# Kernel optimization log

Measured on AMD Instinct MI355X. Metric: run time of the kernel, lower is better.

Reference implementation:

```python
import jax, jax.numpy as jnp
import numpy as np

N_NODES = 100000
N_EDGES = 1600000
N_GRAPHS = 64
IN_F, HID, OUT_F = 10, 128, 101


def setup_inputs() -> dict:
    key = jax.random.key(0)
    ks = jax.random.split(key, 12)
    x = jax.random.normal(ks[0], (N_NODES, IN_F), dtype=jnp.float32)
    edge_index = jax.random.randint(ks[1], (2, N_EDGES), 0, N_NODES, dtype=jnp.int64)
    batch = jnp.sort(jax.random.randint(ks[2], (N_NODES,), 0, N_GRAPHS, dtype=jnp.int64))
    def lin(k, fi, fo):
        s = 1.0 / np.sqrt(fi)
        return jax.random.uniform(k, (fi, fo), minval=-s, maxval=s, dtype=jnp.float32)
    W1 = lin(ks[3], IN_F, HID); b1 = jnp.zeros((HID,), jnp.float32)
    W2 = lin(ks[4], HID, HID); b2 = jnp.zeros((HID,), jnp.float32)
    W3 = lin(ks[5], HID, HID); b3 = jnp.zeros((HID,), jnp.float32)
    Wl = lin(ks[6], HID, OUT_F)
    bl = jax.random.uniform(ks[7], (OUT_F,), minval=-1/np.sqrt(HID), maxval=1/np.sqrt(HID), dtype=jnp.float32)
    return {"x": x, "edge_index": edge_index, "batch": batch,
            "W1": W1, "b1": b1, "W2": W2, "b2": b2, "W3": W3, "b3": b3,
            "Wl": Wl, "bl": bl}


def _gcn_norm(edge_index, n_nodes):
    # Add self-loops and compute symmetric normalization (PyG gcn_norm).
    loop = jnp.arange(n_nodes, dtype=edge_index.dtype)
    src = jnp.concatenate([edge_index[0], loop])
    dst = jnp.concatenate([edge_index[1], loop])
    deg = jax.ops.segment_sum(jnp.ones_like(dst, dtype=jnp.float32), dst, num_segments=n_nodes)
    dis = jnp.where(deg > 0, jax.lax.rsqrt(deg), 0.0)
    w = dis[src] * dis[dst]  # [E + N]
    return src, dst, w


def _gcn_conv(x, W, b, src, dst, w, n_nodes):
    h = x @ W                      # transform first (matches GCNConv)
    msg = h[src] * w[:, None]      # gather + edge normalize
    out = jax.ops.segment_sum(msg, dst, num_segments=n_nodes)  # scatter-add
    return out + b


def reference(x, edge_index, batch, W1, b1, W2, b2, W3, b3, Wl, bl):
    n = x.shape[0]
    src, dst, w = _gcn_norm(edge_index, n)
    h = jax.nn.relu(_gcn_conv(x, W1, b1, src, dst, w, n))
    h = jax.nn.relu(_gcn_conv(h, W2, b2, src, dst, w, n))
    h = _gcn_conv(h, W3, b3, src, dst, w, n)
    # global mean pool per graph
    sums = jax.ops.segment_sum(h, batch, num_segments=N_GRAPHS)
    cnts = jax.ops.segment_sum(jnp.ones((n,), jnp.float32), batch, num_segments=N_GRAPHS)
    pooled = sums / jnp.maximum(cnts, 1.0)[:, None]
    # dropout is identity in eval mode
    return pooled @ Wl + bl
```

## Files before the change

### kernel.cpp

```cpp
#include <hip/hip_runtime.h>
#include <hip/hip_bf16.h>

#define HID 128
#define OUTF 101
#define INF 10
#define XPAD 16

#define BUCK_SHIFT 8
#define NBUCK_MAX 512
#define BCAP 4608
#define FS_EPT 18
#define BS_TPB 256
#define BS_EPT 32
#define BS_EPB (BS_TPB * BS_EPT)

typedef __hip_bfloat16 bf16;
typedef __attribute__((ext_vector_type(8))) short short8;
typedef __attribute__((ext_vector_type(4))) float f32x4;

__device__ __forceinline__ float bflo(unsigned u) { return __uint_as_float(u << 16); }
__device__ __forceinline__ float bfhi(unsigned u) { return __uint_as_float(u & 0xffff0000u); }
__device__ __forceinline__ unsigned pk2(float a, float b) {
    __hip_bfloat162 t;
    t.x = __float2bfloat16(a);
    t.y = __float2bfloat16(b);
    return *reinterpret_cast<unsigned*>(&t);
}


__device__ __forceinline__ void wsplit_body(const float* __restrict__ W, bf16* __restrict__ wfh,
                                            bf16* __restrict__ wfl, int t) {
    int j    = t & 7;
    int lane = (t >> 3) & 63;
    int nt   = (t >> 9) & 7;
    int kb   = t >> 12;
    int k  = kb * 32 + (lane >> 4) * 8 + j;
    int nn = nt * 16 + (lane & 15);
    float w = W[k * HID + nn];
    float hi = __bfloat162float(__float2bfloat16(w));
    wfh[t] = __float2bfloat16(hi);
    wfl[t] = __float2bfloat16(w - hi);
}

__global__ void prep_kernel(const float* __restrict__ x, float* __restrict__ xp, int n,
                            const float* __restrict__ W2, bf16* __restrict__ wf2h,
                            bf16* __restrict__ wf2l,
                            const float* __restrict__ W3, bf16* __restrict__ wf3h,
                            bf16* __restrict__ wf3l,
                            int* __restrict__ gcur, int nbuck,
                            float* __restrict__ sums, int sums_n,
                            int nb_xpad) {
    int b = blockIdx.x;
    int tid = threadIdx.x;
    if (b < nb_xpad) {
        int t = b * 256 + tid;
        if (t < n * XPAD) {
            int i = t >> 4;
            int f = t & 15;
            xp[t] = (f < INF) ? x[(size_t)i * INF + f] : 0.f;
        }
        return;
    }
    b -= nb_xpad;
    if (b < 64) { wsplit_body(W2, wf2h, wf2l, b * 256 + tid); return; }
    b -= 64;
    if (b < 64) { wsplit_body(W3, wf3h, wf3l, b * 256 + tid); return; }
    b -= 64;
    if (b == 0) {
        for (int k = tid; k < nbuck; k += 256) gcur[k] = k * BCAP;
        return;
    }
    b -= 1;
    {
        int t = b * 256 + tid;
        if (t * 4 < sums_n) ((float4*)sums)[t] = make_float4(0.f, 0.f, 0.f, 0.f);
    }
}


__global__ __launch_bounds__(BS_TPB) void bucket_scatter_kernel(
        const int* __restrict__ src, const int* __restrict__ dst, int E,
        int* __restrict__ gcur, int2* __restrict__ estage, int nbuck) {
    __shared__ int cnt[NBUCK_MAX];
    __shared__ int base[NBUCK_MAX];
    int tid = threadIdx.x;
    int e0 = blockIdx.x * BS_EPB + tid;
    int ds[BS_EPT], ss[BS_EPT];
#pragma unroll
    for (int t = 0; t < BS_EPT; ++t) {
        int e = e0 + t * BS_TPB;
        ds[t] = (e < E) ? dst[e] : -1;
        ss[t] = (e < E) ? src[e] : 0;
    }
    for (int b = tid; b < NBUCK_MAX; b += BS_TPB) cnt[b] = 0;
    __syncthreads();
#pragma unroll
    for (int t = 0; t < BS_EPT; ++t)
        if (ds[t] >= 0) atomicAdd(&cnt[ds[t] >> BUCK_SHIFT], 1);
    __syncthreads();
    for (int b = tid; b < nbuck; b += BS_TPB) {
        int c = cnt[b];
        base[b] = c ? atomicAdd(&gcur[b], c) : 0;
    }
    __syncthreads();
    for (int b = tid; b < NBUCK_MAX; b += BS_TPB) cnt[b] = 0;
    __syncthreads();
#pragma unroll
    for (int t = 0; t < BS_EPT; ++t)
        if (ds[t] >= 0) {
            int bk = ds[t] >> BUCK_SHIFT;
            int o = atomicAdd(&cnt[bk], 1);
            estage[base[bk] + o] = make_int2(ss[t], ds[t]);
        }
}

__global__ __launch_bounds__(NBUCK_MAX) void scanb_kernel(const int* __restrict__ gcur,
                                                          int* __restrict__ bbase,
                                                          int* __restrict__ rowp,
                                                          int nbuck, int N) {
    __shared__ int sh[NBUCK_MAX];
    int t = threadIdx.x;
    sh[t] = (t < nbuck) ? (gcur[t] - t * BCAP) : 0;
    __syncthreads();
    for (int off = 1; off < NBUCK_MAX; off <<= 1) {
        int v = (t >= off) ? sh[t - off] : 0;
        __syncthreads();
        sh[t] += v;
        __syncthreads();
    }
    if (t < nbuck) bbase[t] = (t == 0) ? 0 : sh[t - 1];
    if (t == 0) {
        bbase[nbuck] = sh[nbuck - 1];
        rowp[N] = sh[nbuck - 1];
    }
}

__global__ __launch_bounds__(BS_TPB) void fine_scatter_kernel(
        const int2* __restrict__ estage, const int* __restrict__ bbase,
        float* __restrict__ dis, int* __restrict__ rowp,
        int* __restrict__ csrs, int n) {
    __shared__ int hist[256];
    __shared__ int pfx[256];
    __shared__ int lcur[256];
    int b = blockIdx.x;
    int tid = threadIdx.x;
    int node_lo = b << BUCK_SHIFT;
    int bb = bbase[b];
    int cnt = bbase[b + 1] - bb;
    int slo = b * BCAP;
    int2 regs[FS_EPT];
#pragma unroll
    for (int t = 0; t < FS_EPT; ++t) {
        int k = tid + t * BS_TPB;
        regs[t] = (k < cnt) ? estage[slo + k] : make_int2(0, -1);
    }
    hist[tid] = 0;
    __syncthreads();
#pragma unroll
    for (int t = 0; t < FS_EPT; ++t)
        if (regs[t].y >= 0) atomicAdd(&hist[regs[t].y & 255], 1);
    __syncthreads();
    int deg = hist[tid];
    int node = node_lo + tid;
    if (node < n) dis[node] = rsqrtf((float)(deg + 1));
    pfx[tid] = deg;
    __syncthreads();
    for (int off = 1; off < 256; off <<= 1) {
        int v = (tid >= off) ? pfx[tid - off] : 0;
        __syncthreads();
        pfx[tid] += v;
        __syncthreads();
    }
    int excl = (tid == 0) ? 0 : pfx[tid - 1];
    if (node < n) rowp[node] = bb + excl;
    lcur[tid] = excl;
    __syncthreads();
#pragma unroll
    for (int t = 0; t < FS_EPT; ++t)
        if (regs[t].y >= 0) {
            int pos = bb + atomicAdd(&lcur[regs[t].y & 255], 1);
            csrs[pos] = regs[t].x;
        }
}

__global__ __launch_bounds__(256) void aggxform10_kernel(
        const float* __restrict__ xp, const int* __restrict__ rowp,
        const int* __restrict__ csrs, const float* __restrict__ dis,
        const float* __restrict__ W1, const float* __restrict__ b1,
        bf16* __restrict__ h, int n) {
    int i = blockIdx.x * 4 + (threadIdx.x >> 6);
    if (i >= n) return;
    int lane = threadIdx.x & 63;
    int slot = lane >> 4;
    int f = lane & 15;
    float dd = dis[i];

    float acc = (slot == 0) ? xp[(size_t)i * XPAD + f] * dd : 0.f;
    int beg = rowp[i];
    int end = rowp[i + 1];
    for (int base = beg; base < end; base += 4) {
        int e = base + slot;
        int idx = (e < end) ? e : end - 1;
        int s = csrs[idx];
        float w = (e < end) ? dis[s] : 0.f;
        acc = fmaf(xp[(size_t)s * XPAD + f], w, acc);
    }
    acc += __shfl_xor(acc, 16, 64);
    acc += __shfl_xor(acc, 32, 64);
    acc *= dd;

    float axk[INF];
#pragma unroll
    for (int k = 0; k < INF; ++k) axk[k] = __shfl(acc, k, 16);

    int j0 = 2 * lane;
    float2 bb = *(const float2*)(b1 + j0);
    float r0 = bb.x, r1 = bb.y;
#pragma unroll
    for (int k = 0; k < INF; ++k) {
        float2 wv = *(const float2*)(W1 + k * HID + j0);
        r0 = fmaf(axk[k], wv.x, r0);
        r1 = fmaf(axk[k], wv.y, r1);
    }
    r0 = fmaxf(r0, 0.f);
    r1 = fmaxf(r1, 0.f);
    ((unsigned*)(h + (size_t)i * HID))[lane] = pk2(r0, r1);
}


__global__ __launch_bounds__(256) void lin128_mfma_kernel(
        const bf16* __restrict__ in, const bf16* __restrict__ wfh,
        const bf16* __restrict__ wfl, bf16* __restrict__ out, int n) {
    __shared__ short8 wh[2048];
    __shared__ short8 wl[2048];
    for (int v = threadIdx.x; v < 2048; v += 256) {
        wh[v] = ((const short8*)wfh)[v];
        wl[v] = ((const short8*)wfl)[v];
    }
    __syncthreads();

    int lane = threadIdx.x & 63;
    int wave = threadIdx.x >> 6;
    int col = lane & 15;
    int quad = lane >> 4;
    int m0 = blockIdx.x * 128 + wave * 32;

    f32x4 acc[2][8];
#pragma unroll
    for (int mt = 0; mt < 2; ++mt)
#pragma unroll
        for (int nt = 0; nt < 8; ++nt) acc[mt][nt] = (f32x4){0.f, 0.f, 0.f, 0.f};

    long rmax = n - 1;
    long r0 = m0 + col;        if (r0 > rmax) r0 = rmax;
    long r1 = m0 + 16 + col;   if (r1 > rmax) r1 = rmax;

#pragma unroll
    for (int kb = 0; kb < 4; ++kb) {
        int kofs = kb * 32 + quad * 8;
        short8 a0 = *(const short8*)(in + r0 * HID + kofs);
        short8 a1 = *(const short8*)(in + r1 * HID + kofs);
        int bbase = kb * 512 + lane;
#pragma unroll
        for (int nt = 0; nt < 8; ++nt) {
            short8 bh = wh[bbase + nt * 64];
            short8 bl = wl[bbase + nt * 64];
            acc[0][nt] = __builtin_amdgcn_mfma_f32_16x16x32_bf16(a0, bh, acc[0][nt], 0, 0, 0);
            acc[1][nt] = __builtin_amdgcn_mfma_f32_16x16x32_bf16(a1, bh, acc[1][nt], 0, 0, 0);
            acc[0][nt] = __builtin_amdgcn_mfma_f32_16x16x32_bf16(a0, bl, acc[0][nt], 0, 0, 0);
            acc[1][nt] = __builtin_amdgcn_mfma_f32_16x16x32_bf16(a1, bl, acc[1][nt], 0, 0, 0);
        }
    }

#pragma unroll
    for (int mt = 0; mt < 2; ++mt) {
        int mb = m0 + mt * 16 + quad * 4;
#pragma unroll
        for (int r = 0; r < 4; ++r) {
            int m = mb + r;
            if (m < n) {
                bf16* orow = out + (size_t)m * HID + col;
#pragma unroll
                for (int nt = 0; nt < 8; ++nt)
                    orow[nt * 16] = __float2bfloat16(acc[mt][nt][r]);
            }
        }
    }
}

__global__ __launch_bounds__(256) void agg128_kernel(
        const bf16* __restrict__ h, const int* __restrict__ rowp,
        const int* __restrict__ csrs, const float* __restrict__ dis,
        const float* __restrict__ b, bf16* __restrict__ out, int n, int relu) {
    int i = blockIdx.x * 4 + (threadIdx.x >> 6);
    if (i >= n) return;
    int lane = threadIdx.x & 63;
    int slot = lane >> 4;
    int f = lane & 15;
    float dd = dis[i];

    float acc[8];
    if (slot == 0) {
        uint4 v = *(const uint4*)(h + (size_t)i * HID + f * 8);
        acc[0] = bflo(v.x) * dd; acc[1] = bfhi(v.x) * dd;
        acc[2] = bflo(v.y) * dd; acc[3] = bfhi(v.y) * dd;
        acc[4] = bflo(v.z) * dd; acc[5] = bfhi(v.z) * dd;
        acc[6] = bflo(v.w) * dd; acc[7] = bfhi(v.w) * dd;
    } else {
#pragma unroll
        for (int j = 0; j < 8; ++j) acc[j] = 0.f;
    }

    int beg = rowp[i];
    int end = rowp[i + 1];
    for (int base = beg; base < end; base += 8) {
        int e0 = base + slot;
        int e1 = base + 4 + slot;
        int i0 = (e0 < end) ? e0 : end - 1;
        int i1 = (e1 < end) ? e1 : end - 1;
        int s0 = csrs[i0];
        int s1 = csrs[i1];
        float w0 = (e0 < end) ? dis[s0] : 0.f;
        float w1 = (e1 < end) ? dis[s1] : 0.f;
        uint4 v0 = *(const uint4*)(h + (size_t)s0 * HID + f * 8);
        uint4 v1 = *(const uint4*)(h + (size_t)s1 * HID + f * 8);
        acc[0] = fmaf(bflo(v0.x), w0, acc[0]); acc[1] = fmaf(bfhi(v0.x), w0, acc[1]);
        acc[2] = fmaf(bflo(v0.y), w0, acc[2]); acc[3] = fmaf(bfhi(v0.y), w0, acc[3]);
        acc[4] = fmaf(bflo(v0.z), w0, acc[4]); acc[5] = fmaf(bfhi(v0.z), w0, acc[5]);
        acc[6] = fmaf(bflo(v0.w), w0, acc[6]); acc[7] = fmaf(bfhi(v0.w), w0, acc[7]);
        acc[0] = fmaf(bflo(v1.x), w1, acc[0]); acc[1] = fmaf(bfhi(v1.x), w1, acc[1]);
        acc[2] = fmaf(bflo(v1.y), w1, acc[2]); acc[3] = fmaf(bfhi(v1.y), w1, acc[3]);
        acc[4] = fmaf(bflo(v1.z), w1, acc[4]); acc[5] = fmaf(bfhi(v1.z), w1, acc[5]);
        acc[6] = fmaf(bflo(v1.w), w1, acc[6]); acc[7] = fmaf(bfhi(v1.w), w1, acc[7]);
    }

#pragma unroll
    for (int j = 0; j < 8; ++j) {
        acc[j] += __shfl_xor(acc[j], 16, 64);
        acc[j] += __shfl_xor(acc[j], 32, 64);
    }

    float4 b0 = *(const float4*)(b + f * 8);
    float4 b1 = *(const float4*)(b + f * 8 + 4);
    float r[8];
    r[0] = fmaf(acc[0], dd, b0.x); r[1] = fmaf(acc[1], dd, b0.y);
    r[2] = fmaf(acc[2], dd, b0.z); r[3] = fmaf(acc[3], dd, b0.w);
    r[4] = fmaf(acc[4], dd, b1.x); r[5] = fmaf(acc[5], dd, b1.y);
    r[6] = fmaf(acc[6], dd, b1.z); r[7] = fmaf(acc[7], dd, b1.w);
    if (relu) {
#pragma unroll
        for (int j = 0; j < 8; ++j) r[j] = fmaxf(r[j], 0.f);
    }
    if (slot == 0) {
        uint4 pk;
        pk.x = pk2(r[0], r[1]);
        pk.y = pk2(r[2], r[3]);
        pk.z = pk2(r[4], r[5]);
        pk.w = pk2(r[6], r[7]);
        *(uint4*)(out + (size_t)i * HID + f * 8) = pk;
    }
}


__global__ void pool_kernel(const bf16* __restrict__ h, const int* __restrict__ batch, int n,
                            float* __restrict__ sums) {
    int g = blockIdx.x;
    int j = threadIdx.x;
    int lo = 0, hi = n;
    while (lo < hi) { int mid = (lo + hi) >> 1; if (batch[mid] < g) lo = mid + 1; else hi = mid; }
    int start = lo;
    lo = start; hi = n;
    while (lo < hi) { int mid = (lo + hi) >> 1; if (batch[mid] < g + 1) lo = mid + 1; else hi = mid; }
    int end = lo;
    float acc = 0.f;
    for (int i = start + blockIdx.y; i < end; i += gridDim.y)
        acc += __bfloat162float(h[(size_t)i * HID + j]);
    atomicAdd(&sums[g * HID + j], acc);
}

__global__ void final_kernel(const float* __restrict__ sums, const int* __restrict__ batch, int n,
                             const float* __restrict__ Wl, const float* __restrict__ bl,
                             float* __restrict__ out) {
    int g = blockIdx.x;
    int o = threadIdx.x;
    __shared__ float p[HID];
    int lo = 0, hi = n;
    while (lo < hi) { int mid = (lo + hi) >> 1; if (batch[mid] < g) lo = mid + 1; else hi = mid; }
    int start = lo;
    lo = start; hi = n;
    while (lo < hi) { int mid = (lo + hi) >> 1; if (batch[mid] < g + 1) lo = mid + 1; else hi = mid; }
    float cnt = fmaxf((float)(lo - start), 1.0f);
    p[o] = sums[g * HID + o] / cnt;
    __syncthreads();
    if (o < OUTF) {
        float acc = bl[o];
#pragma unroll 8
        for (int k = 0; k < HID; ++k) acc += p[k] * Wl[k * OUTF + o];
        out[g * OUTF + o] = acc;
    }
}


extern "C" void kernel_launch(void* const* d_in, const int* in_sizes, int n_in,
                              void* d_out, int out_size, void* d_ws, size_t ws_size,
                              hipStream_t stream) {
    const float* x   = (const float*)d_in[0];
    const int*   ei  = (const int*)d_in[1];
    const int*   bat = (const int*)d_in[2];
    const float* W1  = (const float*)d_in[3];
    const float* b1  = (const float*)d_in[4];
    const float* W2  = (const float*)d_in[5];
    const float* b2  = (const float*)d_in[6];
    const float* W3  = (const float*)d_in[7];
    const float* b3  = (const float*)d_in[8];
    const float* Wl  = (const float*)d_in[9];
    const float* bl  = (const float*)d_in[10];

    const int N = in_sizes[0] / INF;
    const int E = in_sizes[1] / 2;
    const int G = out_size / OUTF;
    const int* src = ei;
    const int* dst = ei + E;

    const int nbuck = (N + (1 << BUCK_SHIFT) - 1) >> BUCK_SHIFT;

    char* w = (char*)d_ws;
    bf16*  bufA   = (bf16*)w;  w += (size_t)N * HID * 2;
    bf16*  bufB   = (bf16*)w;  w += (size_t)N * HID * 2;
    float* dis    = (float*)w; w += (size_t)N * 4;
    int*   rowp   = (int*)w;   w += (size_t)(N + 8) * 4;
    int*   csrs   = (int*)w;   w += (size_t)E * 4;
    float* sums   = (float*)w; w += (size_t)G * HID * 4;
    int*   gcur   = (int*)w;   w += (size_t)(nbuck + 8) * 4;
    int*   bbase  = (int*)w;   w += (size_t)(nbuck + 8) * 4;
    bf16*  wf2h   = (bf16*)w;  w += (size_t)HID * HID * 2;
    bf16*  wf2l   = (bf16*)w;  w += (size_t)HID * HID * 2;
    bf16*  wf3h   = (bf16*)w;  w += (size_t)HID * HID * 2;
    bf16*  wf3l   = (bf16*)w;  w += (size_t)HID * HID * 2;
    int2*  estage = (int2*)bufA;
    float* xp     = (float*)bufB;

    const int nb_xpad = (N * XPAD + 255) / 256;
    const int sums_n = G * HID;
    prep_kernel<<<nb_xpad + 64 + 64 + 1 + 8, 256, 0, stream>>>(
        x, xp, N, W2, wf2h, wf2l, W3, wf3h, wf3l, gcur, nbuck, sums, sums_n, nb_xpad);

    bucket_scatter_kernel<<<(E + BS_EPB - 1) / BS_EPB, BS_TPB, 0, stream>>>(src, dst, E, gcur,
                                                                            estage, nbuck);
    scanb_kernel<<<1, NBUCK_MAX, 0, stream>>>(gcur, bbase, rowp, nbuck, N);
    fine_scatter_kernel<<<nbuck, BS_TPB, 0, stream>>>(estage, bbase, dis, rowp, csrs, N);

    aggxform10_kernel<<<(N + 3) / 4, 256, 0, stream>>>(xp, rowp, csrs, dis, W1, b1, bufA, N);
    lin128_mfma_kernel<<<(N + 127) / 128, 256, 0, stream>>>(bufA, wf2h, wf2l, bufB, N);
    agg128_kernel<<<(N + 3) / 4, 256, 0, stream>>>(bufB, rowp, csrs, dis, b2, bufA, N, 1);
    lin128_mfma_kernel<<<(N + 127) / 128, 256, 0, stream>>>(bufA, wf3h, wf3l, bufB, N);
    agg128_kernel<<<(N + 3) / 4, 256, 0, stream>>>(bufB, rowp, csrs, dis, b3, bufA, N, 0);

    pool_kernel<<<dim3(G, 32), HID, 0, stream>>>(bufA, bat, N, sums);
    final_kernel<<<G, HID, 0, stream>>>(sums, bat, N, Wl, bl, (float*)d_out);
}
```

Measured before the change: 387.7 us.

## Pre-scale source features by degree norm to drop per-edge dis gathers

Folds the source-side normalization dis[s] into the features before aggregation: x is scaled in fine_scatter and the MFMA output rows are scaled by dis[m]. The aggregation loops can then skip the per-edge dis[s] gather and use plain adds. A zero dummy row at index N replaces masked weights for out-of-range edges. The aggregation loops are also widened (more edges per iteration, float4 loads for the 10-feature layer), and the separate x-padding pass is merged into fine_scatter. The cost is one extra multiply per output element in the linear kernel and slightly larger buffers.

Measured after the change: 356.5 us. 8.1% less time.

```diff
diff --git a/kernel.cpp b/kernel.cpp
--- a/kernel.cpp
+++ b/kernel.cpp
@@ -42,26 +42,17 @@
     wfl[t] = __float2bfloat16(w - hi);
 }
 
-__global__ void prep_kernel(const float* __restrict__ x, float* __restrict__ xp, int n,
-                            const float* __restrict__ W2, bf16* __restrict__ wf2h,
+__global__ void prep_kernel(const float* __restrict__ W2, bf16* __restrict__ wf2h,
                             bf16* __restrict__ wf2l,
                             const float* __restrict__ W3, bf16* __restrict__ wf3h,
                             bf16* __restrict__ wf3l,
                             int* __restrict__ gcur, int nbuck,
                             float* __restrict__ sums, int sums_n,
-                            int nb_xpad) {
+                            float* __restrict__ xps_dummy,
+                            unsigned* __restrict__ hs_dummy)
+{
     int b = blockIdx.x;
     int tid = threadIdx.x;
-    if (b < nb_xpad) {
-        int t = b * 256 + tid;
-        if (t < n * XPAD) {
-            int i = t >> 4;
-            int f = t & 15;
-            xp[t] = (f < INF) ? x[(size_t)i * INF + f] : 0.f;
-        }
-        return;
-    }
-    b -= nb_xpad;
     if (b < 64) { wsplit_body(W2, wf2h, wf2l, b * 256 + tid); return; }
     b -= 64;
     if (b < 64) { wsplit_body(W3, wf3h, wf3l, b * 256 + tid); return; }
@@ -71,10 +62,13 @@
         return;
     }
     b -= 1;
-    {
+    if (b < 8) {
         int t = b * 256 + tid;
         if (t * 4 < sums_n) ((float4*)sums)[t] = make_float4(0.f, 0.f, 0.f, 0.f);
-    }
+        return;
+    }
+    if (tid < XPAD) xps_dummy[tid] = 0.f;
+    if (tid < 64) hs_dummy[tid] = 0u;
 }
 
 
@@ -138,10 +132,12 @@
 __global__ __launch_bounds__(BS_TPB) void fine_scatter_kernel(
         const int2* __restrict__ estage, const int* __restrict__ bbase,
         float* __restrict__ dis, int* __restrict__ rowp,
-        int* __restrict__ csrs, int n) {
+        int* __restrict__ csrs, const float* __restrict__ x,
+        float* __restrict__ xps, int n) {
     __shared__ int hist[256];
     __shared__ int pfx[256];
     __shared__ int lcur[256];
+    __shared__ float sdis[256];
     int b = blockIdx.x;
     int tid = threadIdx.x;
     int node_lo = b << BUCK_SHIFT;
@@ -162,7 +158,9 @@
     __syncthreads();
     int deg = hist[tid];
     int node = node_lo + tid;
-    if (node < n) dis[node] = rsqrtf((float)(deg + 1));
+    float dv = rsqrtf((float)(deg + 1));
+    sdis[tid] = dv;
+    if (node < n) dis[node] = dv;
     pfx[tid] = deg;
     __syncthreads();
     for (int off = 1; off < 256; off <<= 1) {
@@ -181,37 +179,66 @@
             int pos = bb + atomicAdd(&lcur[regs[t].y & 255], 1);
             csrs[pos] = regs[t].x;
         }
+#pragma unroll
+    for (int t = 0; t < 16; ++t) {
+        int idx = tid + t * 256;
+        int nd = node_lo + (idx >> 4);
+        int f = idx & 15;
+        if (nd < n)
+            xps[(size_t)nd * XPAD + f] = (f < INF) ? x[(size_t)nd * INF + f] * sdis[idx >> 4] : 0.f;
+    }
 }
 
 __global__ __launch_bounds__(256) void aggxform10_kernel(
-        const float* __restrict__ xp, const int* __restrict__ rowp,
+        const float* __restrict__ xps, const int* __restrict__ rowp,
         const int* __restrict__ csrs, const float* __restrict__ dis,
         const float* __restrict__ W1, const float* __restrict__ b1,
         bf16* __restrict__ h, int n) {
     int i = blockIdx.x * 4 + (threadIdx.x >> 6);
     if (i >= n) return;
     int lane = threadIdx.x & 63;
-    int slot = lane >> 4;
-    int f = lane & 15;
+    int slot = lane >> 2;
+    int c = lane & 3;
     float dd = dis[i];
 
-    float acc = (slot == 0) ? xp[(size_t)i * XPAD + f] * dd : 0.f;
+    float acc[4];
+    if (slot == 0) {
+        float4 v = *(const float4*)(xps + (size_t)i * XPAD + c * 4);
+        acc[0] = v.x; acc[1] = v.y; acc[2] = v.z; acc[3] = v.w;
+    } else {
+        acc[0] = acc[1] = acc[2] = acc[3] = 0.f;
+    }
+
     int beg = rowp[i];
     int end = rowp[i + 1];
-    for (int base = beg; base < end; base += 4) {
-        int e = base + slot;
-        int idx = (e < end) ? e : end - 1;
-        int s = csrs[idx];
-        float w = (e < end) ? dis[s] : 0.f;
-        acc = fmaf(xp[(size_t)s * XPAD + f], w, acc);
-    }
-    acc += __shfl_xor(acc, 16, 64);
-    acc += __shfl_xor(acc, 32, 64);
-    acc *= dd;
+    for (int base = beg; base < end; base += 32) {
+        int e0 = base + slot;
+        int e1 = base + 16 + slot;
+        int i0 = (e0 < end) ? e0 : end - 1;
+        int i1 = (e1 < end) ? e1 : end - 1;
+        int s0 = csrs[i0];
+        int s1 = csrs[i1];
+        s0 = (e0 < end) ? s0 : n;
+        s1 = (e1 < end) ? s1 : n;
+        float4 v0 = *(const float4*)(xps + (size_t)s0 * XPAD + c * 4);
+        float4 v1 = *(const float4*)(xps + (size_t)s1 * XPAD + c * 4);
+        acc[0] += v0.x + v1.x;
+        acc[1] += v0.y + v1.y;
+        acc[2] += v0.z + v1.z;
+        acc[3] += v0.w + v1.w;
+    }
+#pragma unroll
+    for (int j = 0; j < 4; ++j) {
+        acc[j] += __shfl_xor(acc[j], 4, 64);
+        acc[j] += __shfl_xor(acc[j], 8, 64);
+        acc[j] += __shfl_xor(acc[j], 16, 64);
+        acc[j] += __shfl_xor(acc[j], 32, 64);
+        acc[j] *= dd;
+    }
 
     float axk[INF];
 #pragma unroll
-    for (int k = 0; k < INF; ++k) axk[k] = __shfl(acc, k, 16);
+    for (int k = 0; k < INF; ++k) axk[k] = __shfl(acc[k & 3], k >> 2, 4);
 
     int j0 = 2 * lane;
     float2 bb = *(const float2*)(b1 + j0);
@@ -230,7 +257,8 @@
 
 __global__ __launch_bounds__(256) void lin128_mfma_kernel(
         const bf16* __restrict__ in, const bf16* __restrict__ wfh,
-        const bf16* __restrict__ wfl, bf16* __restrict__ out, int n) {
+        const bf16* __restrict__ wfl, const float* __restrict__ dis,
+        bf16* __restrict__ out, int n) {
     __shared__ short8 wh[2048];
     __shared__ short8 wl[2048];
     for (int v = threadIdx.x; v < 2048; v += 256) {
@@ -279,17 +307,18 @@
         for (int r = 0; r < 4; ++r) {
             int m = mb + r;
             if (m < n) {
+                float dm = dis[m];
                 bf16* orow = out + (size_t)m * HID + col;
 #pragma unroll
                 for (int nt = 0; nt < 8; ++nt)
-                    orow[nt * 16] = __float2bfloat16(acc[mt][nt][r]);
+                    orow[nt * 16] = __float2bfloat16(acc[mt][nt][r] * dm);
             }
         }
     }
 }
 
 __global__ __launch_bounds__(256) void agg128_kernel(
-        const bf16* __restrict__ h, const int* __restrict__ rowp,
+        const bf16* __restrict__ hs, const int* __restrict__ rowp,
         const int* __restrict__ csrs, const float* __restrict__ dis,
         const float* __restrict__ b, bf16* __restrict__ out, int n, int relu) {
     int i = blockIdx.x * 4 + (threadIdx.x >> 6);
@@ -301,11 +330,11 @@
 
     float acc[8];
     if (slot == 0) {
-        uint4 v = *(const uint4*)(h + (size_t)i * HID + f * 8);
-        acc[0] = bflo(v.x) * dd; acc[1] = bfhi(v.x) * dd;
-        acc[2] = bflo(v.y) * dd; acc[3] = bfhi(v.y) * dd;
-        acc[4] = bflo(v.z) * dd; acc[5] = bfhi(v.z) * dd;
-        acc[6] = bflo(v.w) * dd; acc[7] = bfhi(v.w) * dd;
+        uint4 v = *(const uint4*)(hs + (size_t)i * HID + f * 8);
+        acc[0] = bflo(v.x); acc[1] = bfhi(v.x);
+        acc[2] = bflo(v.y); acc[3] = bfhi(v.y);
+        acc[4] = bflo(v.z); acc[5] = bfhi(v.z);
+        acc[6] = bflo(v.w); acc[7] = bfhi(v.w);
     } else {
 #pragma unroll
         for (int j = 0; j < 8; ++j) acc[j] = 0.f;
@@ -313,25 +342,25 @@
 
     int beg = rowp[i];
     int end = rowp[i + 1];
-    for (int base = beg; base < end; base += 8) {
-        int e0 = base + slot;
-        int e1 = base + 4 + slot;
-        int i0 = (e0 < end) ? e0 : end - 1;
-        int i1 = (e1 < end) ? e1 : end - 1;
-        int s0 = csrs[i0];
-        int s1 = csrs[i1];
-        float w0 = (e0 < end) ? dis[s0] : 0.f;
-        float w1 = (e1 < end) ? dis[s1] : 0.f;
-        uint4 v0 = *(const uint4*)(h + (size_t)s0 * HID + f * 8);
-        uint4 v1 = *(const uint4*)(h + (size_t)s1 * HID + f * 8);
-        acc[0] = fmaf(bflo(v0.x), w0, acc[0]); acc[1] = fmaf(bfhi(v0.x), w0, acc[1]);
-        acc[2] = fmaf(bflo(v0.y), w0, acc[2]); acc[3] = fmaf(bfhi(v0.y), w0, acc[3]);
-        acc[4] = fmaf(bflo(v0.z), w0, acc[4]); acc[5] = fmaf(bfhi(v0.z), w0, acc[5]);
-        acc[6] = fmaf(bflo(v0.w), w0, acc[6]); acc[7] = fmaf(bfhi(v0.w), w0, acc[7]);
-        acc[0] = fmaf(bflo(v1.x), w1, acc[0]); acc[1] = fmaf(bfhi(v1.x), w1, acc[1]);
-        acc[2] = fmaf(bflo(v1.y), w1, acc[2]); acc[3] = fmaf(bfhi(v1.y), w1, acc[3]);
-        acc[4] = fmaf(bflo(v1.z), w1, acc[4]); acc[5] = fmaf(bfhi(v1.z), w1, acc[5]);
-        acc[6] = fmaf(bflo(v1.w), w1, acc[6]); acc[7] = fmaf(bfhi(v1.w), w1, acc[7]);
+    for (int base = beg; base < end; base += 16) {
+        int s[4];
+#pragma unroll
+        for (int u = 0; u < 4; ++u) {
+            int e = base + u * 4 + slot;
+            int idx = (e < end) ? e : end - 1;
+            int sv = csrs[idx];
+            s[u] = (e < end) ? sv : n;
+        }
+        uint4 v[4];
+#pragma unroll
+        for (int u = 0; u < 4; ++u) v[u] = *(const uint4*)(hs + (size_t)s[u] * HID + f * 8);
+#pragma unroll
+        for (int u = 0; u < 4; ++u) {
+            acc[0] += bflo(v[u].x); acc[1] += bfhi(v[u].x);
+            acc[2] += bflo(v[u].y); acc[3] += bfhi(v[u].y);
+            acc[4] += bflo(v[u].z); acc[5] += bfhi(v[u].z);
+            acc[6] += bflo(v[u].w); acc[7] += bfhi(v[u].w);
+        }
     }
 
 #pragma unroll
@@ -425,8 +454,8 @@
     const int nbuck = (N + (1 << BUCK_SHIFT) - 1) >> BUCK_SHIFT;
 
     char* w = (char*)d_ws;
-    bf16*  bufA   = (bf16*)w;  w += (size_t)N * HID * 2;
-    bf16*  bufB   = (bf16*)w;  w += (size_t)N * HID * 2;
+    bf16*  bufA   = (bf16*)w;  w += (size_t)(N + 1) * HID * 2;
+    bf16*  bufB   = (bf16*)w;  w += (size_t)(N + 1) * HID * 2;
     float* dis    = (float*)w; w += (size_t)N * 4;
     int*   rowp   = (int*)w;   w += (size_t)(N + 8) * 4;
     int*   csrs   = (int*)w;   w += (size_t)E * 4;
@@ -438,22 +467,22 @@
     bf16*  wf3h   = (bf16*)w;  w += (size_t)HID * HID * 2;
     bf16*  wf3l   = (bf16*)w;  w += (size_t)HID * HID * 2;
     int2*  estage = (int2*)bufA;
-    float* xp     = (float*)bufB;
-
-    const int nb_xpad = (N * XPAD + 255) / 256;
+    float* xps    = (float*)bufB;
+
     const int sums_n = G * HID;
-    prep_kernel<<<nb_xpad + 64 + 64 + 1 + 8, 256, 0, stream>>>(
-        x, xp, N, W2, wf2h, wf2l, W3, wf3h, wf3l, gcur, nbuck, sums, sums_n, nb_xpad);
+    prep_kernel<<<64 + 64 + 1 + 8 + 1, 256, 0, stream>>>(
+        W2, wf2h, wf2l, W3, wf3h, wf3l, gcur, nbuck, sums, sums_n,
+        xps + (size_t)N * XPAD, (unsigned*)(bufB + (size_t)N * HID));
 
     bucket_scatter_kernel<<<(E + BS_EPB - 1) / BS_EPB, BS_TPB, 0, stream>>>(src, dst, E, gcur,
                                                                             estage, nbuck);
     scanb_kernel<<<1, NBUCK_MAX, 0, stream>>>(gcur, bbase, rowp, nbuck, N);
-    fine_scatter_kernel<<<nbuck, BS_TPB, 0, stream>>>(estage, bbase, dis, rowp, csrs, N);
-
-    aggxform10_kernel<<<(N + 3) / 4, 256, 0, stream>>>(xp, rowp, csrs, dis, W1, b1, bufA, N);
-    lin128_mfma_kernel<<<(N + 127) / 128, 256, 0, stream>>>(bufA, wf2h, wf2l, bufB, N);
+    fine_scatter_kernel<<<nbuck, BS_TPB, 0, stream>>>(estage, bbase, dis, rowp, csrs, x, xps, N);
+
+    aggxform10_kernel<<<(N + 3) / 4, 256, 0, stream>>>(xps, rowp, csrs, dis, W1, b1, bufA, N);
+    lin128_mfma_kernel<<<(N + 127) / 128, 256, 0, stream>>>(bufA, wf2h, wf2l, dis, bufB, N);
     agg128_kernel<<<(N + 3) / 4, 256, 0, stream>>>(bufB, rowp, csrs, dis, b2, bufA, N, 1);
-    lin128_mfma_kernel<<<(N + 127) / 128, 256, 0, stream>>>(bufA, wf3h, wf3l, bufB, N);
+    lin128_mfma_kernel<<<(N + 127) / 128, 256, 0, stream>>>(bufA, wf3h, wf3l, dis, bufB, N);
     agg128_kernel<<<(N + 3) / 4, 256, 0, stream>>>(bufB, rowp, csrs, dis, b3, bufA, N, 0);
 
     pool_kernel<<<dim3(G, 32), HID, 0, stream>>>(bufA, bat, N, sums);
```
